# Kernel tuning notes

Measured on AMD Instinct MI355X. Metric: run time of the kernel, lower is better.

## Reference

```python
import jax, jax.numpy as jnp
import numpy as np

N_NODES = 100000
N_EDGES = 1600000
D_IN = 128
HIDDEN = 128
D_OUT = 40
EPS = 1e-12  # F.normalize eps


def _glorot(key, shape):
    lim = float(np.sqrt(6.0 / (shape[0] + shape[1])))
    return jax.random.uniform(key, shape, jnp.float32, -lim, lim)


def setup_inputs() -> dict:
    key = jax.random.key(0)
    ks = jax.random.split(key, 8)
    x = jax.random.normal(ks[0], (N_NODES, D_IN), jnp.float32)
    edge_index = jax.random.randint(ks[1], (2, N_EDGES), 0, N_NODES, jnp.int64)
    return {
        "x": x,
        "edge_index": edge_index,
        "W_l1": _glorot(ks[2], (D_IN, HIDDEN)),
        "b_l1": jnp.zeros((HIDDEN,), jnp.float32),
        "W_r1": _glorot(ks[3], (D_IN, HIDDEN)),
        "W_l2": _glorot(ks[4], (HIDDEN, D_OUT)),
        "b_l2": jnp.zeros((D_OUT,), jnp.float32),
        "W_r2": _glorot(ks[5], (HIDDEN, D_OUT)),
    }


def _sage_conv(x, src, dst, W_l, b_l, W_r):
    # mean aggregation of source-node features into destination nodes
    n = x.shape[0]
    summed = jax.ops.segment_sum(x[src], dst, num_segments=n)          # [N, d]
    deg = jax.ops.segment_sum(jnp.ones_like(dst, x.dtype), dst, num_segments=n)
    mean = summed / jnp.maximum(deg, 1.0)[:, None]
    out = mean @ W_l + b_l + x @ W_r                                   # [N, d_out]
    # normalize=True: L2 row-normalize
    norm = jnp.maximum(jnp.linalg.norm(out, axis=-1, keepdims=True), EPS)
    return out / norm


def reference(x, edge_index, W_l1, b_l1, W_r1, W_l2, b_l2, W_r2):
    src, dst = edge_index[0], edge_index[1]
    # dropout p=0.6 is identity at inference (training=False)
    h = jax.nn.relu(_sage_conv(x, src, dst, W_l1, b_l1, W_r1))
    out = _sage_conv(h, src, dst, W_l2, b_l2, W_r2)
    return jax.nn.log_softmax(out, axis=1)
```

## Files before the change

kernel.cpp:

```cpp
#include <hip/hip_runtime.h>
#include <math.h>

#define N_NODES 100000
#define N_EDGES 1600000
#define D_IN 128
#define HIDDEN 128
#define D_OUT 40
#define EPSN 1e-12f

#define NBUCK 391
#define EPB 4096
#define NPART ((N_EDGES + EPB - 1) / EPB)
#define PEPB 16384
#define PNPART ((N_EDGES + PEPB - 1) / PEPB)

#define SWZ1_TOTAL (8 * 8 * 4 * 16 * 8)
#define SWZ2_TOTAL (4 * 8 * 4 * 16 * 8)
#define CASTB ((N_NODES * 16) / 256)
#define F8B ((N_NODES * 32) / 256)
#define SWZB ((SWZ1_TOTAL + SWZ2_TOTAL + 255) / 256)

typedef __attribute__((ext_vector_type(8))) short short8;
typedef __attribute__((ext_vector_type(4))) float float4v;
typedef __attribute__((ext_vector_type(2))) float float2v;

static __device__ inline unsigned short f2bf(float f) {
    union { float f; unsigned u; } v; v.f = f;
    unsigned r = v.u + 0x7fffu + ((v.u >> 16) & 1u);
    return (unsigned short)(r >> 16);
}
static __device__ inline float bflo(unsigned u) {
    union { unsigned u; float f; } v; v.u = u << 16;
    return v.f;
}
static __device__ inline float bfhi(unsigned u) {
    union { unsigned u; float f; } v; v.u = u & 0xffff0000u;
    return v.f;
}

#if defined(__has_builtin)
#if __has_builtin(__builtin_amdgcn_cvt_pk_f32_fp8) && __has_builtin(__builtin_amdgcn_cvt_pk_fp8_f32)
#define HAVE_HW_FP8 1
#endif
#endif

static __device__ inline float2v fp8lo(unsigned u) {
#ifdef HAVE_HW_FP8
    return __builtin_amdgcn_cvt_pk_f32_fp8(u, false);
#else
    unsigned b0 = u & 0xffu, b1 = (u >> 8) & 0xffu;
    union { unsigned u; float f; } v0, v1;
    v0.u = ((b0 & 0x80u) << 24) | ((b0 & 0x7fu) << 20);
    v1.u = ((b1 & 0x80u) << 24) | ((b1 & 0x7fu) << 20);
    float2v r; r.x = v0.f * 0x1p+120f; r.y = v1.f * 0x1p+120f;
    return r;
#endif
}
static __device__ inline float2v fp8hi(unsigned u) {
#ifdef HAVE_HW_FP8
    return __builtin_amdgcn_cvt_pk_f32_fp8(u, true);
#else
    unsigned b0 = (u >> 16) & 0xffu, b1 = (u >> 24) & 0xffu;
    union { unsigned u; float f; } v0, v1;
    v0.u = ((b0 & 0x80u) << 24) | ((b0 & 0x7fu) << 20);
    v1.u = ((b1 & 0x80u) << 24) | ((b1 & 0x7fu) << 20);
    float2v r; r.x = v0.f * 0x1p+120f; r.y = v1.f * 0x1p+120f;
    return r;
#endif
}
#ifndef HAVE_HW_FP8
static __device__ inline unsigned enc1(float x) {
    union { float f; unsigned u; } v; v.f = x * 0x1p-120f;
    unsigned um = v.u & 0x7fffffffu;
    unsigned r = um + 0x7FFFFu + ((um >> 20) & 1u);
    return ((r >> 20) & 0x7fu) | ((v.u >> 24) & 0x80u);
}
#endif
static __device__ inline unsigned fp8pack(float f0, float f1, float f2, float f3) {
#ifdef HAVE_HW_FP8
    unsigned u = __builtin_amdgcn_cvt_pk_fp8_f32(f0, f1, 0u, false);
    u = __builtin_amdgcn_cvt_pk_fp8_f32(f2, f3, u, true);
    return u;
#else
    return enc1(f0) | (enc1(f1) << 8) | (enc1(f2) << 16) | (enc1(f3) << 24);
#endif
}

__global__ void prep_kernel(const int* __restrict__ dst, int* __restrict__ bucketCount,
                            const float* __restrict__ x, unsigned* __restrict__ xb,
                            unsigned* __restrict__ xf8,
                            const float* __restrict__ Wl1, const float* __restrict__ Wr1,
                            const float* __restrict__ Wl2, const float* __restrict__ Wr2,
                            unsigned short* __restrict__ out1, unsigned short* __restrict__ out2) {
    __shared__ int h[NBUCK];
    int b = blockIdx.x, t = threadIdx.x;
    if (b < NPART) {
        for (int i = t; i < NBUCK; i += 256) h[i] = 0;
        __syncthreads();
        int es = b * EPB;
        int ee = min(es + EPB, N_EDGES);
        for (int i = es + t; i < ee; i += 256) atomicAdd(&h[dst[i] >> 8], 1);
        __syncthreads();
        for (int i = t; i < NBUCK; i += 256)
            if (h[i]) atomicAdd(&bucketCount[i], h[i]);
        return;
    }
    b -= NPART;
    if (b < CASTB) {
        int g = b * 256 + t;
        const float4* x4 = (const float4*)x;
        float4 lo = x4[2 * g], hi = x4[2 * g + 1];
        uint4 o;
        o.x = (unsigned)f2bf(lo.x) | ((unsigned)f2bf(lo.y) << 16);
        o.y = (unsigned)f2bf(lo.z) | ((unsigned)f2bf(lo.w) << 16);
        o.z = (unsigned)f2bf(hi.x) | ((unsigned)f2bf(hi.y) << 16);
        o.w = (unsigned)f2bf(hi.z) | ((unsigned)f2bf(hi.w) << 16);
        ((uint4*)xb)[g] = o;
        return;
    }
    b -= CASTB;
    if (b < F8B) {
        int g = b * 256 + t;
        float4 f = ((const float4*)x)[g];
        xf8[g] = fp8pack(f.x, f.y, f.z, f.w);
        return;
    }
    b -= F8B;
    {
        int idx = b * 256 + t;
        if (idx < SWZ1_TOTAL) {
            int j = idx & 7, l15 = (idx >> 3) & 15, quad = (idx >> 7) & 3;
            int rem = idx >> 9;
            int c = rem & 7, kt = rem >> 3;
            int k = kt * 32 + quad * 8 + j;
            int n = c * 16 + l15;
            float val = (k < 128) ? Wl1[k * HIDDEN + n] : Wr1[(k - 128) * HIDDEN + n];
            out1[idx] = f2bf(val);
        } else if (idx < SWZ1_TOTAL + SWZ2_TOTAL) {
            idx -= SWZ1_TOTAL;
            int j = idx & 7, l15 = (idx >> 3) & 15, quad = (idx >> 7) & 3;
            int rem = idx >> 9;
            int c = rem & 7, kt = rem >> 3;
            int k = kt * 32 + quad * 8 + j;
            int n = c * 16 + l15;
            float val = 0.0f;
            if (n < D_OUT) val = Wl2[k * D_OUT + n];
            else if (n >= 64 && n < 64 + D_OUT) val = Wr2[k * D_OUT + (n - 64)];
            out2[idx] = f2bf(val);
        }
    }
}

__global__ void bscan_kernel(const int* __restrict__ bc, int* __restrict__ bstart,
                             int* __restrict__ cursor) {
    __shared__ int s[256];
    int t = threadIdx.x;
    int a = (2 * t < NBUCK) ? bc[2 * t] : 0;
    int b = (2 * t + 1 < NBUCK) ? bc[2 * t + 1] : 0;
    int tp = a + b;
    s[t] = tp;
    __syncthreads();
    for (int off = 1; off < 256; off <<= 1) {
        int tmp = (t >= off) ? s[t - off] : 0;
        __syncthreads();
        s[t] += tmp;
        __syncthreads();
    }
    int texcl = s[t] - tp;
    if (2 * t < NBUCK) { bstart[2 * t] = texcl; cursor[2 * t] = texcl; }
    if (2 * t + 1 < NBUCK) { bstart[2 * t + 1] = texcl + a; cursor[2 * t + 1] = texcl + a; }
    if (t == 255) bstart[NBUCK] = s[255];
}

__global__ __launch_bounds__(512) void bpart_kernel(
    const int* __restrict__ src, const int* __restrict__ dst,
    int* __restrict__ cursor, unsigned* __restrict__ pairs) {
    __shared__ int h[NBUCK];
    __shared__ int base[NBUCK];
    int t = threadIdx.x;
    for (int i = t; i < NBUCK; i += 512) h[i] = 0;
    __syncthreads();
    int es = blockIdx.x * PEPB;
    int ee = min(es + PEPB, N_EDGES);
    for (int i = es + t; i < ee; i += 512) atomicAdd(&h[dst[i] >> 8], 1);
    __syncthreads();
    for (int i = t; i < NBUCK; i += 512) {
        int c = h[i];
        base[i] = c ? atomicAdd(&cursor[i], c) : 0;
    }
    __syncthreads();
    for (int i = t; i < NBUCK; i += 512) h[i] = 0;
    __syncthreads();
    for (int i = es + t; i < ee; i += 512) {
        int d = dst[i];
        int bk = d >> 8;
        int r = atomicAdd(&h[bk], 1);
        pairs[base[bk] + r] = ((unsigned)src[i] << 8) | (unsigned)(d & 255);
    }
}

__global__ void csr_kernel(const unsigned* __restrict__ pairs, const int* __restrict__ bstart,
                           int* __restrict__ hist, int* __restrict__ rowStart,
                           int* __restrict__ sortedSrc) {
    __shared__ int cnt[256];
    __shared__ int sc[256];
    __shared__ int cur[256];
    int b = blockIdx.x, t = threadIdx.x;
    int es = bstart[b], ee = bstart[b + 1];
    cnt[t] = 0;
    __syncthreads();
    for (int i = es + t; i < ee; i += 256) atomicAdd(&cnt[pairs[i] & 255], 1);
    __syncthreads();
    int v = cnt[t];
    sc[t] = v;
    __syncthreads();
    for (int off = 1; off < 256; off <<= 1) {
        int tmp = (t >= off) ? sc[t - off] : 0;
        __syncthreads();
        sc[t] += tmp;
        __syncthreads();
    }
    int excl = sc[t] - v;
    int node = (b << 8) + t;
    if (node < N_NODES) {
        hist[node] = v;
        rowStart[node] = es + excl;
    }
    cur[t] = excl;
    __syncthreads();
    for (int i = es + t; i < ee; i += 256) {
        unsigned p = pairs[i];
        int r = atomicAdd(&cur[p & 255], 1);
        sortedSrc[es + r] = (int)(p >> 8);
    }
}

#define ACC4(v)                                                                   \
    { float2v p;                                                                  \
      p = fp8lo(v.x); a[0] += p.x; a[1] += p.y;                                   \
      p = fp8hi(v.x); a[2] += p.x; a[3] += p.y;                                   \
      p = fp8lo(v.y); a[4] += p.x; a[5] += p.y;                                   \
      p = fp8hi(v.y); a[6] += p.x; a[7] += p.y;                                   \
      p = fp8lo(v.z); a[8] += p.x; a[9] += p.y;                                   \
      p = fp8hi(v.z); a[10] += p.x; a[11] += p.y;                                 \
      p = fp8lo(v.w); a[12] += p.x; a[13] += p.y;                                 \
      p = fp8hi(v.w); a[14] += p.x; a[15] += p.y; }

__global__ void agg_kernel(const uint4* __restrict__ xf8,
                           const int* __restrict__ sortedSrc,
                           const int* __restrict__ rowStart, const int* __restrict__ hist,
                           uint4* __restrict__ meanb) {
    int w = __builtin_amdgcn_readfirstlane((int)(threadIdx.x >> 6));
    int node = blockIdx.x * 4 + w;
    int lane = threadIdx.x & 63;
    int q = lane >> 3, sl = lane & 7;
    int s0 = __builtin_amdgcn_readfirstlane(rowStart[node]);
    int cnt = __builtin_amdgcn_readfirstlane(hist[node]);
    float a[16];
#pragma unroll
    for (int e = 0; e < 16; e++) a[e] = 0.f;
    int i = 0;
    for (; i + 16 <= cnt; i += 16) {
        int sA = sortedSrc[s0 + i + q];
        int sB = sortedSrc[s0 + i + 8 + q];
        uint4 vA = xf8[(size_t)sA * 8 + sl];
        uint4 vB = xf8[(size_t)sB * 8 + sl];
        ACC4(vA)
        ACC4(vB)
    }
    for (; i + 8 <= cnt; i += 8) {
        int s = sortedSrc[s0 + i + q];
        uint4 v = xf8[(size_t)s * 8 + sl];
        ACC4(v)
    }
    if (q < cnt - i) {
        int s = sortedSrc[s0 + i + q];
        uint4 v = xf8[(size_t)s * 8 + sl];
        ACC4(v)
    }
#pragma unroll
    for (int e = 0; e < 16; e++) {
        a[e] += __shfl_xor(a[e], 8, 64);
        a[e] += __shfl_xor(a[e], 16, 64);
        a[e] += __shfl_xor(a[e], 32, 64);
    }
    if (q == 0) {
        float dinv = 1.0f / fmaxf((float)cnt, 1.0f);
        uint4 o1, o2;
        o1.x = (unsigned)f2bf(a[0] * dinv)  | ((unsigned)f2bf(a[1] * dinv) << 16);
        o1.y = (unsigned)f2bf(a[2] * dinv)  | ((unsigned)f2bf(a[3] * dinv) << 16);
        o1.z = (unsigned)f2bf(a[4] * dinv)  | ((unsigned)f2bf(a[5] * dinv) << 16);
        o1.w = (unsigned)f2bf(a[6] * dinv)  | ((unsigned)f2bf(a[7] * dinv) << 16);
        o2.x = (unsigned)f2bf(a[8] * dinv)  | ((unsigned)f2bf(a[9] * dinv) << 16);
        o2.y = (unsigned)f2bf(a[10] * dinv) | ((unsigned)f2bf(a[11] * dinv) << 16);
        o2.z = (unsigned)f2bf(a[12] * dinv) | ((unsigned)f2bf(a[13] * dinv) << 16);
        o2.w = (unsigned)f2bf(a[14] * dinv) | ((unsigned)f2bf(a[15] * dinv) << 16);
        meanb[(size_t)node * 16 + sl * 2] = o1;
        meanb[(size_t)node * 16 + sl * 2 + 1] = o2;
    }
}

__global__ __launch_bounds__(256) void gemm1g_kernel(
    const unsigned short* __restrict__ meanb, const unsigned short* __restrict__ xb,
    const short* __restrict__ bswz1, const float* __restrict__ bias1,
    const short* __restrict__ bswz2,
    unsigned short* __restrict__ g_l, unsigned short* __restrict__ g_r) {
    __shared__ unsigned short hT[4][16][140];
    int tid = threadIdx.x;
    int w = __builtin_amdgcn_readfirstlane(tid >> 6);
    int lane = tid & 63;
    int l15 = lane & 15, quad = lane >> 4;
    int n0 = blockIdx.x * 64;
    int nodeA = n0 + w * 16 + l15;
    if (nodeA >= N_NODES) nodeA = N_NODES - 1;

    float4v acc[8];
#pragma unroll
    for (int c = 0; c < 8; c++) acc[c] = (float4v){0.f, 0.f, 0.f, 0.f};
#pragma unroll
    for (int kt = 0; kt < 8; kt++) {
        const unsigned short* ab = (kt < 4) ? meanb : xb;
        short8 a = *(const short8*)(ab + (size_t)nodeA * 128 + (kt & 3) * 32 + quad * 8);
#pragma unroll
        for (int c = 0; c < 8; c++) {
            short8 b = *(const short8*)(bswz1 + (((kt * 8 + c) * 4 + quad) * 16 + l15) * 8);
            acc[c] = __builtin_amdgcn_mfma_f32_16x16x32_bf16(a, b, acc[c], 0, 0, 0);
        }
    }

    float v[8][4];
    float ss[4] = {0.f, 0.f, 0.f, 0.f};
#pragma unroll
    for (int c = 0; c < 8; c++) {
        float bi = bias1[c * 16 + l15];
#pragma unroll
        for (int r = 0; r < 4; r++) {
            float t = acc[c][r] + bi;
            v[c][r] = t;
            ss[r] += t * t;
        }
    }
#pragma unroll
    for (int r = 0; r < 4; r++)
        for (int off = 1; off < 16; off <<= 1) ss[r] += __shfl_xor(ss[r], off, 64);
#pragma unroll
    for (int r = 0; r < 4; r++) {
        float inv = 1.0f / fmaxf(sqrtf(ss[r]), EPSN);
#pragma unroll
        for (int c = 0; c < 8; c++) {
            hT[w][quad * 4 + r][c * 16 + l15] = f2bf(fmaxf(v[c][r] * inv, 0.0f));
        }
    }

    float4v acc2[8];
#pragma unroll
    for (int c = 0; c < 8; c++) acc2[c] = (float4v){0.f, 0.f, 0.f, 0.f};
#pragma unroll
    for (int kt = 0; kt < 4; kt++) {
        short8 a = *(const short8*)&hT[w][l15][kt * 32 + quad * 8];
#pragma unroll
        for (int c = 0; c < 8; c++) {
            short8 b = *(const short8*)(bswz2 + (((kt * 8 + c) * 4 + quad) * 16 + l15) * 8);
            acc2[c] = __builtin_amdgcn_mfma_f32_16x16x32_bf16(a, b, acc2[c], 0, 0, 0);
        }
    }
#pragma unroll
    for (int r = 0; r < 4; r++) {
        int node = n0 + w * 16 + quad * 4 + r;
        if (node < N_NODES) {
#pragma unroll
            for (int c = 0; c < 4; c++)
                g_l[(size_t)node * 64 + c * 16 + l15] = f2bf(acc2[c][r]);
#pragma unroll
            for (int c = 4; c < 8; c++)
                g_r[(size_t)node * 64 + (c - 4) * 16 + l15] = f2bf(acc2[c][r]);
        }
    }
}

__global__ void fused2h_kernel(const uint4* __restrict__ g_l4, const uint4* __restrict__ g_r4,
                               const int* __restrict__ sortedSrc,
                               const int* __restrict__ rowStart, const int* __restrict__ hist,
                               const float* __restrict__ bias, float* __restrict__ out) {
    int tid = threadIdx.x;
    int w = __builtin_amdgcn_readfirstlane(tid >> 6);
    int lane = tid & 63;
    int g = lane >> 4, q1 = (lane >> 3) & 1, sl = lane & 7;
    int node = blockIdx.x * 16 + w * 4 + g;
    int s0 = rowStart[node];
    int cnt = hist[node];
    float a0 = 0.f, a1 = 0.f, a2 = 0.f, a3 = 0.f, a4 = 0.f, a5 = 0.f, a6 = 0.f, a7 = 0.f;
    int i = 0;
    for (; i + 4 <= cnt; i += 4) {
        int sA = sortedSrc[s0 + i + q1];
        int sB = sortedSrc[s0 + i + 2 + q1];
        uint4 vA = g_l4[(size_t)sA * 8 + sl];
        uint4 vB = g_l4[(size_t)sB * 8 + sl];
        a0 += bflo(vA.x) + bflo(vB.x); a1 += bfhi(vA.x) + bfhi(vB.x);
        a2 += bflo(vA.y) + bflo(vB.y); a3 += bfhi(vA.y) + bfhi(vB.y);
        a4 += bflo(vA.z) + bflo(vB.z); a5 += bfhi(vA.z) + bfhi(vB.z);
        a6 += bflo(vA.w) + bflo(vB.w); a7 += bfhi(vA.w) + bfhi(vB.w);
    }
    if (i + q1 < cnt) {
        int s = sortedSrc[s0 + i + q1];
        uint4 v = g_l4[(size_t)s * 8 + sl];
        a0 += bflo(v.x); a1 += bfhi(v.x); a2 += bflo(v.y); a3 += bfhi(v.y);
        a4 += bflo(v.z); a5 += bfhi(v.z); a6 += bflo(v.w); a7 += bfhi(v.w);
    }
    i += 2;
    if (i + q1 < cnt) {
        int s = sortedSrc[s0 + i + q1];
        uint4 v = g_l4[(size_t)s * 8 + sl];
        a0 += bflo(v.x); a1 += bfhi(v.x); a2 += bflo(v.y); a3 += bfhi(v.y);
        a4 += bflo(v.z); a5 += bfhi(v.z); a6 += bflo(v.w); a7 += bfhi(v.w);
    }
    a0 += __shfl_xor(a0, 8, 64);
    a1 += __shfl_xor(a1, 8, 64);
    a2 += __shfl_xor(a2, 8, 64);
    a3 += __shfl_xor(a3, 8, 64);
    a4 += __shfl_xor(a4, 8, 64);
    a5 += __shfl_xor(a5, 8, 64);
    a6 += __shfl_xor(a6, 8, 64);
    a7 += __shfl_xor(a7, 8, 64);
    float dinv = 1.0f / fmaxf((float)cnt, 1.0f);
    uint4 gr = g_r4[(size_t)node * 8 + sl];
    bool valid = (sl < 5);
    float b0 = 0, b1 = 0, b2 = 0, b3 = 0, b4 = 0, b5 = 0, b6 = 0, b7 = 0;
    if (valid) {
        b0 = bias[sl * 8 + 0]; b1 = bias[sl * 8 + 1]; b2 = bias[sl * 8 + 2]; b3 = bias[sl * 8 + 3];
        b4 = bias[sl * 8 + 4]; b5 = bias[sl * 8 + 5]; b6 = bias[sl * 8 + 6]; b7 = bias[sl * 8 + 7];
    }
    float t0 = a0 * dinv + bflo(gr.x) + b0;
    float t1 = a1 * dinv + bfhi(gr.x) + b1;
    float t2 = a2 * dinv + bflo(gr.y) + b2;
    float t3 = a3 * dinv + bfhi(gr.y) + b3;
    float t4 = a4 * dinv + bflo(gr.z) + b4;
    float t5 = a5 * dinv + bfhi(gr.z) + b5;
    float t6 = a6 * dinv + bflo(gr.w) + b6;
    float t7 = a7 * dinv + bfhi(gr.w) + b7;
    float ssq = t0 * t0 + t1 * t1 + t2 * t2 + t3 * t3 + t4 * t4 + t5 * t5 + t6 * t6 + t7 * t7;
    ssq += __shfl_xor(ssq, 1, 64); ssq += __shfl_xor(ssq, 2, 64); ssq += __shfl_xor(ssq, 4, 64);
    float inv = 1.0f / fmaxf(sqrtf(ssq), EPSN);
    float v0 = t0 * inv, v1 = t1 * inv, v2 = t2 * inv, v3 = t3 * inv;
    float v4 = t4 * inv, v5 = t5 * inv, v6 = t6 * inv, v7 = t7 * inv;
    float m = valid ? fmaxf(fmaxf(fmaxf(v0, v1), fmaxf(v2, v3)),
                            fmaxf(fmaxf(v4, v5), fmaxf(v6, v7))) : -INFINITY;
    m = fmaxf(m, __shfl_xor(m, 1, 64));
    m = fmaxf(m, __shfl_xor(m, 2, 64));
    m = fmaxf(m, __shfl_xor(m, 4, 64));
    float se = 0.0f;
    if (valid) {
        se = expf(v0 - m) + expf(v1 - m) + expf(v2 - m) + expf(v3 - m) +
             expf(v4 - m) + expf(v5 - m) + expf(v6 - m) + expf(v7 - m);
    }
    se += __shfl_xor(se, 1, 64); se += __shfl_xor(se, 2, 64); se += __shfl_xor(se, 4, 64);
    float ls = logf(se) + m;
    if (q1 == 0 && valid) {
        float* o = out + (size_t)node * D_OUT + sl * 8;
        ((float4*)o)[0] = (float4){v0 - ls, v1 - ls, v2 - ls, v3 - ls};
        ((float4*)o)[1] = (float4){v4 - ls, v5 - ls, v6 - ls, v7 - ls};
    }
}

static inline size_t align256(size_t x) { return (x + 255) & ~(size_t)255; }

extern "C" void kernel_launch(void* const* d_in, const int* in_sizes, int n_in,
                              void* d_out, int out_size, void* d_ws, size_t ws_size,
                              hipStream_t stream) {
    const float* x   = (const float*)d_in[0];
    const int*   ei  = (const int*)d_in[1];
    const float* Wl1 = (const float*)d_in[2];
    const float* bl1 = (const float*)d_in[3];
    const float* Wr1 = (const float*)d_in[4];
    const float* Wl2 = (const float*)d_in[5];
    const float* bl2 = (const float*)d_in[6];
    const float* Wr2 = (const float*)d_in[7];
    float* out = (float*)d_out;

    const int* src = ei;
    const int* dst = ei + N_EDGES;

    char* ws = (char*)d_ws;
    size_t off = 0;
    int* bucketCount = (int*)(ws + off); off += align256((size_t)NBUCK * 4);
    int* bucketStart = (int*)(ws + off); off += align256((size_t)(NBUCK + 1) * 4);
    int* cursor      = (int*)(ws + off); off += align256((size_t)NBUCK * 4);
    int* hist        = (int*)(ws + off); off += align256((size_t)N_NODES * 4);
    int* rowStart    = (int*)(ws + off); off += align256((size_t)N_NODES * 4);
    unsigned* pairs  = (unsigned*)(ws + off); off += align256((size_t)N_EDGES * 4);
    int* sortedSrc   = (int*)(ws + off); off += align256((size_t)N_EDGES * 4);
    unsigned* xb     = (unsigned*)(ws + off); off += align256((size_t)N_NODES * 128 * 2);
    unsigned* xf8    = (unsigned*)(ws + off); off += align256((size_t)N_NODES * 128);
    unsigned* meanb  = (unsigned*)(ws + off); off += align256((size_t)N_NODES * 128 * 2);
    unsigned short* g_l = (unsigned short*)(ws + off); off += align256((size_t)N_NODES * 64 * 2);
    unsigned short* g_r = (unsigned short*)(ws + off); off += align256((size_t)N_NODES * 64 * 2);
    unsigned short* bswz1 = (unsigned short*)(ws + off); off += align256((size_t)SWZ1_TOTAL * 2);
    unsigned short* bswz2 = (unsigned short*)(ws + off); off += align256((size_t)SWZ2_TOTAL * 2);

    hipMemsetAsync(bucketCount, 0, (size_t)NBUCK * 4, stream);

    prep_kernel<<<NPART + CASTB + F8B + SWZB, 256, 0, stream>>>(
        dst, bucketCount, x, xb, xf8, Wl1, Wr1, Wl2, Wr2, bswz1, bswz2);
    bscan_kernel<<<1, 256, 0, stream>>>(bucketCount, bucketStart, cursor);
    bpart_kernel<<<PNPART, 512, 0, stream>>>(src, dst, cursor, pairs);
    csr_kernel<<<NBUCK, 256, 0, stream>>>(pairs, bucketStart, hist, rowStart, sortedSrc);

    agg_kernel<<<N_NODES / 4, 256, 0, stream>>>((const uint4*)xf8, sortedSrc, rowStart, hist,
                                                (uint4*)meanb);
    gemm1g_kernel<<<(N_NODES + 63) / 64, 256, 0, stream>>>(
        (const unsigned short*)meanb, (const unsigned short*)xb,
        (const short*)bswz1, bl1, (const short*)bswz2, g_l, g_r);
    fused2h_kernel<<<N_NODES / 16, 256, 0, stream>>>(
        (const uint4*)g_l, (const uint4*)g_r, sortedSrc, rowStart, hist, bl2, out);
}
```

Measured before the change: 304.3 us.

## Fuse fp8 cast into bf16 cast blocks and regroup aggregation lanes

```diff
diff --git a/kernel.cpp b/kernel.cpp
--- a/kernel.cpp
+++ b/kernel.cpp
@@ -17,7 +17,6 @@
 #define SWZ1_TOTAL (8 * 8 * 4 * 16 * 8)
 #define SWZ2_TOTAL (4 * 8 * 4 * 16 * 8)
 #define CASTB ((N_NODES * 16) / 256)
-#define F8B ((N_NODES * 32) / 256)
 #define SWZB ((SWZ1_TOTAL + SWZ2_TOTAL + 255) / 256)
 
 typedef __attribute__((ext_vector_type(8))) short short8;
@@ -116,16 +115,13 @@
         o.z = (unsigned)f2bf(hi.x) | ((unsigned)f2bf(hi.y) << 16);
         o.w = (unsigned)f2bf(hi.z) | ((unsigned)f2bf(hi.w) << 16);
         ((uint4*)xb)[g] = o;
+        uint2 o8;
+        o8.x = fp8pack(lo.x, lo.y, lo.z, lo.w);
+        o8.y = fp8pack(hi.x, hi.y, hi.z, hi.w);
+        ((uint2*)xf8)[g] = o8;
         return;
     }
     b -= CASTB;
-    if (b < F8B) {
-        int g = b * 256 + t;
-        float4 f = ((const float4*)x)[g];
-        xf8[g] = fp8pack(f.x, f.y, f.z, f.w);
-        return;
-    }
-    b -= F8B;
     {
         int idx = b * 256 + t;
         if (idx < SWZ1_TOTAL) {
@@ -235,68 +231,61 @@
     }
 }
 
-#define ACC4(v)                                                                   \
-    { float2v p;                                                                  \
-      p = fp8lo(v.x); a[0] += p.x; a[1] += p.y;                                   \
-      p = fp8hi(v.x); a[2] += p.x; a[3] += p.y;                                   \
-      p = fp8lo(v.y); a[4] += p.x; a[5] += p.y;                                   \
-      p = fp8hi(v.y); a[6] += p.x; a[7] += p.y;                                   \
-      p = fp8lo(v.z); a[8] += p.x; a[9] += p.y;                                   \
-      p = fp8hi(v.z); a[10] += p.x; a[11] += p.y;                                 \
-      p = fp8lo(v.w); a[12] += p.x; a[13] += p.y;                                 \
-      p = fp8hi(v.w); a[14] += p.x; a[15] += p.y; }
-
-__global__ void agg_kernel(const uint4* __restrict__ xf8,
+#define ACC2(v)                                                                   \
+    { a[0] += fp8lo(v.x); a[1] += fp8hi(v.x);                                     \
+      a[2] += fp8lo(v.y); a[3] += fp8hi(v.y); }
+
+__global__ void agg_kernel(const uint2* __restrict__ xf8,
                            const int* __restrict__ sortedSrc,
                            const int* __restrict__ rowStart, const int* __restrict__ hist,
                            uint4* __restrict__ meanb) {
     int w = __builtin_amdgcn_readfirstlane((int)(threadIdx.x >> 6));
     int node = blockIdx.x * 4 + w;
     int lane = threadIdx.x & 63;
-    int q = lane >> 3, sl = lane & 7;
+    int g = lane >> 4, sl = lane & 15;
     int s0 = __builtin_amdgcn_readfirstlane(rowStart[node]);
     int cnt = __builtin_amdgcn_readfirstlane(hist[node]);
-    float a[16];
-#pragma unroll
-    for (int e = 0; e < 16; e++) a[e] = 0.f;
+    float2v a[4];
+#pragma unroll
+    for (int e = 0; e < 4; e++) a[e] = (float2v){0.f, 0.f};
     int i = 0;
-    for (; i + 16 <= cnt; i += 16) {
-        int sA = sortedSrc[s0 + i + q];
-        int sB = sortedSrc[s0 + i + 8 + q];
-        uint4 vA = xf8[(size_t)sA * 8 + sl];
-        uint4 vB = xf8[(size_t)sB * 8 + sl];
-        ACC4(vA)
-        ACC4(vB)
-    }
     for (; i + 8 <= cnt; i += 8) {
-        int s = sortedSrc[s0 + i + q];
-        uint4 v = xf8[(size_t)s * 8 + sl];
-        ACC4(v)
-    }
-    if (q < cnt - i) {
-        int s = sortedSrc[s0 + i + q];
-        uint4 v = xf8[(size_t)s * 8 + sl];
-        ACC4(v)
-    }
-#pragma unroll
-    for (int e = 0; e < 16; e++) {
-        a[e] += __shfl_xor(a[e], 8, 64);
-        a[e] += __shfl_xor(a[e], 16, 64);
-        a[e] += __shfl_xor(a[e], 32, 64);
-    }
-    if (q == 0) {
+        int sA = sortedSrc[s0 + i + g];
+        int sB = sortedSrc[s0 + i + 4 + g];
+        uint2 vA = xf8[sA * 16 + sl];
+        uint2 vB = xf8[sB * 16 + sl];
+        ACC2(vA)
+        ACC2(vB)
+    }
+    if (i + 4 <= cnt) {
+        int s = sortedSrc[s0 + i + g];
+        uint2 v = xf8[s * 16 + sl];
+        ACC2(v)
+        i += 4;
+    }
+    if (g < cnt - i) {
+        int s = sortedSrc[s0 + i + g];
+        uint2 v = xf8[s * 16 + sl];
+        ACC2(v)
+    }
+#pragma unroll
+    for (int e = 0; e < 4; e++) {
+        a[e].x += __shfl_xor(a[e].x, 16, 64);
+        a[e].y += __shfl_xor(a[e].y, 16, 64);
+    }
+#pragma unroll
+    for (int e = 0; e < 4; e++) {
+        a[e].x += __shfl_xor(a[e].x, 32, 64);
+        a[e].y += __shfl_xor(a[e].y, 32, 64);
+    }
+    if (g == 0) {
         float dinv = 1.0f / fmaxf((float)cnt, 1.0f);
-        uint4 o1, o2;
-        o1.x = (unsigned)f2bf(a[0] * dinv)  | ((unsigned)f2bf(a[1] * dinv) << 16);
-        o1.y = (unsigned)f2bf(a[2] * dinv)  | ((unsigned)f2bf(a[3] * dinv) << 16);
-        o1.z = (unsigned)f2bf(a[4] * dinv)  | ((unsigned)f2bf(a[5] * dinv) << 16);
-        o1.w = (unsigned)f2bf(a[6] * dinv)  | ((unsigned)f2bf(a[7] * dinv) << 16);
-        o2.x = (unsigned)f2bf(a[8] * dinv)  | ((unsigned)f2bf(a[9] * dinv) << 16);
-        o2.y = (unsigned)f2bf(a[10] * dinv) | ((unsigned)f2bf(a[11] * dinv) << 16);
-        o2.z = (unsigned)f2bf(a[12] * dinv) | ((unsigned)f2bf(a[13] * dinv) << 16);
-        o2.w = (unsigned)f2bf(a[14] * dinv) | ((unsigned)f2bf(a[15] * dinv) << 16);
-        meanb[(size_t)node * 16 + sl * 2] = o1;
-        meanb[(size_t)node * 16 + sl * 2 + 1] = o2;
+        uint4 o;
+        o.x = (unsigned)f2bf(a[0].x * dinv) | ((unsigned)f2bf(a[0].y * dinv) << 16);
+        o.y = (unsigned)f2bf(a[1].x * dinv) | ((unsigned)f2bf(a[1].y * dinv) << 16);
+        o.z = (unsigned)f2bf(a[2].x * dinv) | ((unsigned)f2bf(a[2].y * dinv) << 16);
+        o.w = (unsigned)f2bf(a[3].x * dinv) | ((unsigned)f2bf(a[3].y * dinv) << 16);
+        meanb[node * 16 + sl] = o;
     }
 }
 
@@ -499,13 +488,13 @@
 
     hipMemsetAsync(bucketCount, 0, (size_t)NBUCK * 4, stream);
 
-    prep_kernel<<<NPART + CASTB + F8B + SWZB, 256, 0, stream>>>(
+    prep_kernel<<<NPART + CASTB + SWZB, 256, 0, stream>>>(
         dst, bucketCount, x, xb, xf8, Wl1, Wr1, Wl2, Wr2, bswz1, bswz2);
     bscan_kernel<<<1, 256, 0, stream>>>(bucketCount, bucketStart, cursor);
     bpart_kernel<<<PNPART, 512, 0, stream>>>(src, dst, cursor, pairs);
     csr_kernel<<<NBUCK, 256, 0, stream>>>(pairs, bucketStart, hist, rowStart, sortedSrc);
 
-    agg_kernel<<<N_NODES / 4, 256, 0, stream>>>((const uint4*)xf8, sortedSrc, rowStart, hist,
+    agg_kernel<<<N_NODES / 4, 256, 0, stream>>>((const uint2*)xf8, sortedSrc, rowStart, hist,
                                                 (uint4*)meanb);
     gemm1g_kernel<<<(N_NODES + 63) / 64, 256, 0, stream>>>(
         (const unsigned short*)meanb, (const unsigned short*)xb,
```

New measurement: 292.4 us. 3.9% less time.
